# Optimization experiments

Measured on AMD Instinct MI355X. Metric: run time of the kernel, lower is better.

## Reference

```python
import jax, jax.numpy as jnp
import numpy as np

INF8 = 255
H, D = 8, 64  # num_heads, head dim (hidden=512)
G = 1         # num_global_node


def setup_inputs() -> dict:
    key = jax.random.key(0)
    ks = jax.random.split(key, 12)
    B, N, HID = 8, 1023, 512
    S = N + G
    inp = {
        'q': jax.random.normal(ks[0], (B, S, HID), jnp.float32),
        'k': jax.random.normal(ks[1], (B, S, HID), jnp.float32),
        'v': jax.random.normal(ks[2], (B, S, HID), jnp.float32),
        'attn_bias': jax.random.randint(ks[3], (B, N, N, 1), 0, 255).astype(jnp.int32),
        'Wq': 0.02 * jax.random.normal(ks[4], (HID, HID), jnp.float32),
        'bq': jnp.zeros((HID,), jnp.float32),
        'Wk': 0.02 * jax.random.normal(ks[5], (HID, HID), jnp.float32),
        'bk': jnp.zeros((HID,), jnp.float32),
        'Wv': 0.02 * jax.random.normal(ks[6], (HID, HID), jnp.float32),
        'bv': jnp.zeros((HID,), jnp.float32),
        'Wo': 0.02 * jax.random.normal(ks[7], (HID, HID), jnp.float32),
        'bo': jnp.zeros((HID,), jnp.float32),
        'bias_table': 0.02 * jax.random.normal(ks[8], (INF8 + 1, H), jnp.float32),
        'vbias': 0.02 * jax.random.normal(ks[9], (G, H), jnp.float32),
    }
    return inp


def _structural_bias(attn_bias, bias_table, vbias):
    # attn_bias: [B, N, N, 1] int -> [B, H, N+G, N+G] float
    ab = attn_bias[..., 0]                      # [B,N,N]
    B, N, _ = ab.shape
    bias = bias_table[ab]                       # [B,N,N,H]
    mask = ab == INF8
    bias = jnp.where(mask[..., None], -jnp.inf, bias)
    row = jnp.broadcast_to(vbias[None, :, None, :], (B, G, N, bias.shape[-1]))
    bias = jnp.concatenate([bias, row], axis=1)             # [B,N+G,N,H]
    col = jnp.broadcast_to(vbias[None, None, :, :], (B, N + G, G, bias.shape[-1]))
    bias = jnp.concatenate([bias, col], axis=2)             # [B,N+G,N+G,H]
    return bias.transpose(0, 3, 1, 2)                       # [B,H,S,S]


def reference(q, k, v, attn_bias, Wq, bq, Wk, bk, Wv, bv, Wo, bo, bias_table, vbias):
    B, S, HID = q.shape
    scale = D ** -0.5
    qh = (q @ Wq.T + bq).reshape(B, S, H, D)
    kh = (k @ Wk.T + bk).reshape(B, S, H, D)
    vh = (v @ Wv.T + bv).reshape(B, S, H, D)
    scores = jnp.einsum('bshd,bthd->bhst', qh * scale, kh)  # [B,H,S,S]
    scores = scores + _structural_bias(attn_bias, bias_table, vbias)
    p = jax.nn.softmax(scores, axis=-1)
    # dropout is identity in eval mode
    ctx = jnp.einsum('bhst,bthd->bshd', p, vh).reshape(B, S, HID)
    return ctx @ Wo.T + bo
```

## Files before the change

### kernel.cpp

```cpp
#include <hip/hip_runtime.h>
#include <hip/hip_bf16.h>


typedef __attribute__((ext_vector_type(8)))  __bf16 bf16x8;
typedef __attribute__((ext_vector_type(16))) float  f32x16;

__device__ inline f32x16 zero16(){
  f32x16 z;
  #pragma unroll
  for (int i=0;i<16;i++) z[i] = 0.0f;
  return z;
}

__device__ inline unsigned short f2bf(float x){
  unsigned u = __float_as_uint(x);
  u += 0x7fffu + ((u>>16)&1u);
  return (unsigned short)(u>>16);
}
__device__ inline unsigned f2bf_pair(float a, float b){
  unsigned ua = __float_as_uint(a); ua += 0x7fffu + ((ua>>16)&1u);
  unsigned ub = __float_as_uint(b); ub += 0x7fffu + ((ub>>16)&1u);
  return (ua>>16) | (ub & 0xffff0000u);
}
__device__ inline unsigned comb2(unsigned a, unsigned b, float rn){
  const float a0 = __uint_as_float(a<<16), a1 = __uint_as_float(a & 0xffff0000u);
  const float b0 = __uint_as_float(b<<16), b1 = __uint_as_float(b & 0xffff0000u);
  return f2bf_pair((a0+b0)*rn, (a1+b1)*rn);
}

__device__ inline void bar_lgkm(){
  asm volatile("s_waitcnt lgkmcnt(0)" ::: "memory");
  __builtin_amdgcn_s_barrier();
}

__global__ __launch_bounds__(256)
void ab_transpose(const int* ab, unsigned short* abT)
{
  __shared__ int tl[64*65];
  const int k  = blockIdx.x;
  const int b  = k >> 8;
  const int ti = k & 255;
  const int t0 = (ti & 15) << 6, q0 = (ti >> 4) << 6;
  const int c  = threadIdx.x & 63, r0 = threadIdx.x >> 6;
  #pragma unroll
  for (int rp = 0; rp < 16; ++rp){
    const int r = r0 + rp*4;
    const int q = q0 + r, t = t0 + c;
    int v = 256;
    if (q < 1023 && t < 1023) v = ab[((size_t)b*1023 + q)*1023 + t];
    tl[r*65 + c] = v;
  }
  __syncthreads();
  unsigned short* dst = abT + ((size_t)b << 20);
  #pragma unroll
  for (int rp = 0; rp < 16; ++rp){
    const int r = r0 + rp*4;
    dst[(size_t)(t0 + r)*1024 + q0 + c] = (unsigned short)tl[c*65 + r];
  }
}

__global__ __launch_bounds__(256)
void qkv_proj(const float* xq, const float* xk, const float* xv,
              const float* Wq, const float* Wk, const float* Wv,
              const float* bq, const float* bk, const float* bv,
              unsigned short* qh, unsigned short* kh, unsigned short* vht2,
              float scaleq)
{
  __shared__ unsigned short lda[128*40];
  __shared__ unsigned short ldb[128*40];
  const int bid = blockIdx.x;
  const int sel = bid >> 8;
  const int t   = bid & 255;
  const float *RA, *RB, *bias;
  int r0, c0;
  if (sel == 0){ RA = xq; RB = Wq; bias = bq; r0 = (t&63)*128; c0 = (t>>6)*128; }
  else if (sel == 1){ RA = xk; RB = Wk; bias = bk; r0 = (t&63)*128; c0 = (t>>6)*128; }
  else { RA = Wv; RB = xv; bias = bv; r0 = (t&3)*128; c0 = (t>>2)*128; }

  const int tid  = threadIdx.x;
  const int w    = tid>>6, lane = tid&63, lo = lane&31, hi = lane>>5;
  const int wr   = (w>>1)*64, wc = (w&1)*64;
  const int arow = tid>>1, kb = (tid&1)*16;

  f32x16 acc[2][2];
  #pragma unroll
  for (int i=0;i<2;i++)
    #pragma unroll
    for (int j=0;j<2;j++) acc[i][j] = zero16();

  float4 ra[4], rb4[4];
  {
    const float4* p = (const float4*)(RA + (r0+arow)*512 + kb);
    ra[0]=p[0]; ra[1]=p[1]; ra[2]=p[2]; ra[3]=p[3];
    const float4* pq = (const float4*)(RB + (c0+arow)*512 + kb);
    rb4[0]=pq[0]; rb4[1]=pq[1]; rb4[2]=pq[2]; rb4[3]=pq[3];
  }

  for (int ks=0; ks<16; ++ks){
    bar_lgkm();
    {
      uint4 w0, w1;
      w0.x = f2bf_pair(ra[0].x, ra[0].y); w0.y = f2bf_pair(ra[0].z, ra[0].w);
      w0.z = f2bf_pair(ra[1].x, ra[1].y); w0.w = f2bf_pair(ra[1].z, ra[1].w);
      w1.x = f2bf_pair(ra[2].x, ra[2].y); w1.y = f2bf_pair(ra[2].z, ra[2].w);
      w1.z = f2bf_pair(ra[3].x, ra[3].y); w1.w = f2bf_pair(ra[3].z, ra[3].w);
      uint4* pa = (uint4*)&lda[arow*40 + kb];
      pa[0] = w0; pa[1] = w1;
      uint4 v0, v1;
      v0.x = f2bf_pair(rb4[0].x, rb4[0].y); v0.y = f2bf_pair(rb4[0].z, rb4[0].w);
      v0.z = f2bf_pair(rb4[1].x, rb4[1].y); v0.w = f2bf_pair(rb4[1].z, rb4[1].w);
      v1.x = f2bf_pair(rb4[2].x, rb4[2].y); v1.y = f2bf_pair(rb4[2].z, rb4[2].w);
      v1.z = f2bf_pair(rb4[3].x, rb4[3].y); v1.w = f2bf_pair(rb4[3].z, rb4[3].w);
      uint4* pb = (uint4*)&ldb[arow*40 + kb];
      pb[0] = v0; pb[1] = v1;
    }
    if (ks < 15){
      const int k0 = (ks+1)*32;
      const float4* p = (const float4*)(RA + (r0+arow)*512 + k0 + kb);
      ra[0]=p[0]; ra[1]=p[1]; ra[2]=p[2]; ra[3]=p[3];
      const float4* pq = (const float4*)(RB + (c0+arow)*512 + k0 + kb);
      rb4[0]=pq[0]; rb4[1]=pq[1]; rb4[2]=pq[2]; rb4[3]=pq[3];
    }
    bar_lgkm();
    #pragma unroll
    for (int kf=0; kf<2; ++kf){
      bf16x8 af0 = *(const bf16x8*)&lda[(wr+lo)*40    + kf*16 + hi*8];
      bf16x8 af1 = *(const bf16x8*)&lda[(wr+32+lo)*40 + kf*16 + hi*8];
      bf16x8 bg0 = *(const bf16x8*)&ldb[(wc+lo)*40    + kf*16 + hi*8];
      bf16x8 bg1 = *(const bf16x8*)&ldb[(wc+32+lo)*40 + kf*16 + hi*8];
      acc[0][0] = __builtin_amdgcn_mfma_f32_32x32x16_bf16(af0, bg0, acc[0][0], 0,0,0);
      acc[0][1] = __builtin_amdgcn_mfma_f32_32x32x16_bf16(af0, bg1, acc[0][1], 0,0,0);
      acc[1][0] = __builtin_amdgcn_mfma_f32_32x32x16_bf16(af1, bg0, acc[1][0], 0,0,0);
      acc[1][1] = __builtin_amdgcn_mfma_f32_32x32x16_bf16(af1, bg1, acc[1][1], 0,0,0);
    }
  }

  #pragma unroll
  for (int mi=0;mi<2;mi++){
    #pragma unroll
    for (int ni=0;ni<2;ni++){
      #pragma unroll
      for (int r=0;r<16;r++){
        const int rl = wr + mi*32 + (r&3) + 8*(r>>2) + 4*hi;
        const int cl = wc + ni*32 + lo;
        const int rg = r0 + rl, cg = c0 + cl;
        float v = acc[mi][ni][r];
        if (sel == 0){
          v = (v + bias[cg]) * scaleq;
          const int bb = rg>>10, s = rg&1023, h = cg>>6, d = cg&63;
          qh[(((bb*8+h)*1024)+s)*64 + d] = f2bf(v);
        } else if (sel == 1){
          v = v + bias[cg];
          const int bb = rg>>10, s = rg&1023, h = cg>>6, d = cg&63;
          kh[(((bb*8+h)*1024)+s)*64 + d] = f2bf(v);
        } else {
          v = v + bias[rg];
          const int h = rg>>6, d = rg&63, bb = cg>>10, s = cg&1023;
          vht2[(((size_t)(bb*8+h)*32 + (s>>5))*64 + d)*32 + (s&31)] = f2bf(v);
        }
      }
    }
  }
}

__global__ __launch_bounds__(256)
void out_proj(const unsigned short* ctx0, const unsigned short* ctx1,
              const float* lsump, const float* Wo, const float* bo, float* OUT)
{
  __shared__ unsigned short lda[128*40];
  __shared__ unsigned short ldb[128*40];
  const int tid  = threadIdx.x;
  const int r0   = blockIdx.x*128, c0 = blockIdx.y*128;
  const int w    = tid>>6, lane = tid&63, lo = lane&31, hi = lane>>5;
  const int wr   = (w>>1)*64, wc = (w&1)*64;
  const int arow = tid>>1, kb = (tid&1)*16;
  const int rgs  = r0 + arow, bb = rgs>>10, ss = rgs&1023;
  const float* lb0 = lsump + (size_t)(bb*8)*1024 + ss;
  const float* lb1 = lsump + (size_t)((8+bb)*8)*1024 + ss;

  f32x16 acc[2][2];
  #pragma unroll
  for (int i=0;i<2;i++)
    #pragma unroll
    for (int j=0;j<2;j++) acc[i][j] = zero16();

  uint4 ra0[2], ra1[2];
  float4 rb4[4];
  float l0, l1;

  {
    const uint4* p0 = (const uint4*)(ctx0 + rgs*512 + kb);
    ra0[0]=p0[0]; ra0[1]=p0[1];
    const uint4* p1 = (const uint4*)(ctx1 + rgs*512 + kb);
    ra1[0]=p1[0]; ra1[1]=p1[1];
    const int h = kb>>6;
    l0 = lb0[h*1024]; l1 = lb1[h*1024];
    const float4* pq = (const float4*)(Wo + (c0+arow)*512 + kb);
    rb4[0]=pq[0]; rb4[1]=pq[1]; rb4[2]=pq[2]; rb4[3]=pq[3];
  }

  for (int ks=0; ks<16; ++ks){
    bar_lgkm();
    {
      const float rn = __builtin_amdgcn_rcpf(l0 + l1);
      uint4 w0, w1;
      w0.x = comb2(ra0[0].x, ra1[0].x, rn); w0.y = comb2(ra0[0].y, ra1[0].y, rn);
      w0.z = comb2(ra0[0].z, ra1[0].z, rn); w0.w = comb2(ra0[0].w, ra1[0].w, rn);
      w1.x = comb2(ra0[1].x, ra1[1].x, rn); w1.y = comb2(ra0[1].y, ra1[1].y, rn);
      w1.z = comb2(ra0[1].z, ra1[1].z, rn); w1.w = comb2(ra0[1].w, ra1[1].w, rn);
      uint4* pa = (uint4*)&lda[arow*40 + kb];
      pa[0] = w0; pa[1] = w1;
      uint4 v0, v1;
      v0.x = f2bf_pair(rb4[0].x, rb4[0].y); v0.y = f2bf_pair(rb4[0].z, rb4[0].w);
      v0.z = f2bf_pair(rb4[1].x, rb4[1].y); v0.w = f2bf_pair(rb4[1].z, rb4[1].w);
      v1.x = f2bf_pair(rb4[2].x, rb4[2].y); v1.y = f2bf_pair(rb4[2].z, rb4[2].w);
      v1.z = f2bf_pair(rb4[3].x, rb4[3].y); v1.w = f2bf_pair(rb4[3].z, rb4[3].w);
      uint4* pb = (uint4*)&ldb[arow*40 + kb];
      pb[0] = v0; pb[1] = v1;
    }
    if (ks < 15){
      const int k0 = (ks+1)*32;
      const uint4* p0 = (const uint4*)(ctx0 + rgs*512 + k0 + kb);
      ra0[0]=p0[0]; ra0[1]=p0[1];
      const uint4* p1 = (const uint4*)(ctx1 + rgs*512 + k0 + kb);
      ra1[0]=p1[0]; ra1[1]=p1[1];
      const int h = (k0+kb)>>6;
      l0 = lb0[h*1024]; l1 = lb1[h*1024];
      const float4* pq = (const float4*)(Wo + (c0+arow)*512 + k0 + kb);
      rb4[0]=pq[0]; rb4[1]=pq[1]; rb4[2]=pq[2]; rb4[3]=pq[3];
    }
    bar_lgkm();
    #pragma unroll
    for (int kf=0; kf<2; ++kf){
      bf16x8 af0 = *(const bf16x8*)&lda[(wr+lo)*40    + kf*16 + hi*8];
      bf16x8 af1 = *(const bf16x8*)&lda[(wr+32+lo)*40 + kf*16 + hi*8];
      bf16x8 bg0 = *(const bf16x8*)&ldb[(wc+lo)*40    + kf*16 + hi*8];
      bf16x8 bg1 = *(const bf16x8*)&ldb[(wc+32+lo)*40 + kf*16 + hi*8];
      acc[0][0] = __builtin_amdgcn_mfma_f32_32x32x16_bf16(af0, bg0, acc[0][0], 0,0,0);
      acc[0][1] = __builtin_amdgcn_mfma_f32_32x32x16_bf16(af0, bg1, acc[0][1], 0,0,0);
      acc[1][0] = __builtin_amdgcn_mfma_f32_32x32x16_bf16(af1, bg0, acc[1][0], 0,0,0);
      acc[1][1] = __builtin_amdgcn_mfma_f32_32x32x16_bf16(af1, bg1, acc[1][1], 0,0,0);
    }
  }

  #pragma unroll
  for (int mi=0;mi<2;mi++){
    #pragma unroll
    for (int ni=0;ni<2;ni++){
      #pragma unroll
      for (int r=0;r<16;r++){
        const int rl = wr + mi*32 + (r&3) + 8*(r>>2) + 4*hi;
        const int cl = wc + ni*32 + lo;
        const int rg = r0 + rl, cg = c0 + cl;
        OUT[rg*512 + cg] = acc[mi][ni][r] + bo[cg];
      }
    }
  }
}

__global__ __launch_bounds__(256)
void attn_fused(const unsigned short* qh, const unsigned short* kh,
                const unsigned short* vht2, const unsigned short* abT,
                const float* bias_table, const float* vbias,
                unsigned short* ctxp, float* lsump)
{
  __shared__ float tbl[260];
  __shared__ unsigned short kls[32*72];
  __shared__ unsigned short vls[64*40];
  __shared__ unsigned short abls[32*136];

  const int tid = threadIdx.x;
  const int m   = blockIdx.x;
  const int sg  = m >> 7;
  const int c   = m & 127;
  const int h   = c & 7;
  const int ts  = (c >> 3) & 1;
  const int b   = c >> 4;
  const int tb  = ts*512;
  const int q0  = sg*128;

  for (int i = tid; i < 257; i += 256){
    float v;
    if (i < 255)       v = bias_table[i*8 + h];
    else if (i == 255) v = -1.0e30f;
    else               v = vbias[h];
    tbl[i] = v * 1.4426950408889634f;
  }

  const int w = tid>>6, lane = tid&63, lo = lane&31, hi = lane>>5;
  const bool hib = (hi != 0);
  const int s0 = q0 + w*32;

  const unsigned short* qbase  = qh   + (size_t)(b*8+h)*65536;
  const unsigned short* kbase  = kh   + (size_t)(b*8+h)*65536 + (size_t)tb*64;
  const unsigned short* vbase  = vht2 + ((size_t)(b*8+h)*32 + (tb>>5))*2048;
  const unsigned short* abbase = abT  + ((size_t)b<<20) + q0;

  bf16x8 qf[4];
  #pragma unroll
  for (int kf=0; kf<4; ++kf)
    qf[kf] = *(const bf16x8*)&qbase[(s0+lo)*64 + kf*16 + hi*8];

  f32x16 accv[2]; accv[0] = zero16(); accv[1] = zero16();
  float lsum = 0.0f;

  const int kdst = (tid>>3)*72  + (tid&7)*8;
  const int vdst = (tid>>2)*40  + (tid&3)*8;
  const int adst = (tid>>3)*136 + (tid&7)*16;

  uint4 krg, vrg, ar0, ar1;
  krg = *(const uint4*)&kbase[tid*8];
  vrg = *(const uint4*)&vbase[tid*8];
  ar0 = *(const uint4*)&abbase[(size_t)(tb + (tid>>3))*1024 + (tid&7)*16];
  ar1 = *(const uint4*)&abbase[(size_t)(tb + (tid>>3))*1024 + (tid&7)*16 + 8];

  for (int tt=0; tt<512; tt+=32){
    bar_lgkm();
    *(uint4*)&kls[kdst]    = krg;
    *(uint4*)&vls[vdst]    = vrg;
    *(uint4*)&abls[adst]   = ar0;
    *(uint4*)&abls[adst+8] = ar1;
    {
      const int tn = (tt+32)&511;
      krg = *(const uint4*)&kbase[tn*64 + tid*8];
      vrg = *(const uint4*)&vbase[(tn>>5)*2048 + tid*8];
      ar0 = *(const uint4*)&abbase[(size_t)(tb + tn + (tid>>3))*1024 + (tid&7)*16];
      ar1 = *(const uint4*)&abbase[(size_t)(tb + tn + (tid>>3))*1024 + (tid&7)*16 + 8];
    }
    bar_lgkm();

    f32x16 sc = zero16();
    #pragma unroll
    for (int kf=0; kf<4; ++kf){
      bf16x8 kfr = *(const bf16x8*)&kls[lo*72 + kf*16 + hi*8];
      sc = __builtin_amdgcn_mfma_f32_32x32x16_bf16(kfr, qf[kf], sc, 0,0,0);
    }

    unsigned d[4][2];
    float ls = 0.0f;
    #pragma unroll
    for (int g=0; g<4; ++g){
      float p[4];
      #pragma unroll
      for (int u=0; u<4; ++u){
        const int crow = u + 8*g + 4*hi;
        const int idx  = abls[crow*136 + w*32 + lo];
        p[u] = __builtin_amdgcn_exp2f(sc[4*g+u] + tbl[idx]);
        ls  += p[u];
      }
      d[g][0] = f2bf_pair(p[0], p[1]);
      d[g][1] = f2bf_pair(p[2], p[3]);
    }
    lsum += ls;

    unsigned x[4][2];
    #pragma unroll
    for (int g=0; g<4; ++g){
      x[g][0] = __shfl_xor(d[g][0], 32, 64);
      x[g][1] = __shfl_xor(d[g][1], 32, 64);
    }

    #pragma unroll
    for (int c2=0; c2<2; ++c2){
      union { unsigned u[4]; bf16x8 v; } pc;
      pc.u[0] = hib ? x[2*c2+1][0] : d[2*c2][0];
      pc.u[1] = hib ? x[2*c2+1][1] : d[2*c2][1];
      pc.u[2] = hib ? d[2*c2+1][0] : x[2*c2][0];
      pc.u[3] = hib ? d[2*c2+1][1] : x[2*c2][1];
      bf16x8 vf0 = *(const bf16x8*)&vls[(     lo)*40 + c2*16 + hi*8];
      bf16x8 vf1 = *(const bf16x8*)&vls[(32 + lo)*40 + c2*16 + hi*8];
      accv[0] = __builtin_amdgcn_mfma_f32_32x32x16_bf16(pc.v, vf0, accv[0], 0,0,0);
      accv[1] = __builtin_amdgcn_mfma_f32_32x32x16_bf16(pc.v, vf1, accv[1], 0,0,0);
    }
  }

  lsum += __shfl_xor(lsum, 32, 64);

  unsigned short* cbase = ctxp + (size_t)ts*4194304;
  #pragma unroll
  for (int dc=0; dc<2; ++dc){
    #pragma unroll
    for (int r=0;r<16;r++){
      const int rq = (r&3) + 8*(r>>2) + 4*hi;
      cbase[((size_t)b*1024 + s0 + rq)*512 + h*64 + dc*32 + lo] = f2bf(accv[dc][r]);
    }
  }
  if (hi == 0){
    lsump[((size_t)(ts*8 + b)*8 + h)*1024 + s0 + lo] = lsum;
  }
}

extern "C" void kernel_launch(void* const* d_in, const int* in_sizes, int n_in,
                              void* d_out, int out_size, void* d_ws, size_t ws_size,
                              hipStream_t stream)
{
  const float* q    = (const float*)d_in[0];
  const float* k    = (const float*)d_in[1];
  const float* v    = (const float*)d_in[2];
  const int*   ab   = (const int*)  d_in[3];
  const float* Wq   = (const float*)d_in[4];
  const float* bq   = (const float*)d_in[5];
  const float* Wk   = (const float*)d_in[6];
  const float* bk   = (const float*)d_in[7];
  const float* Wv   = (const float*)d_in[8];
  const float* bv   = (const float*)d_in[9];
  const float* Wo   = (const float*)d_in[10];
  const float* bo   = (const float*)d_in[11];
  const float* btab = (const float*)d_in[12];
  const float* vbia = (const float*)d_in[13];

  char* ws = (char*)d_ws;
  unsigned short* qh   = (unsigned short*)(ws);
  unsigned short* kh   = (unsigned short*)(ws + ((size_t) 8<<20));
  unsigned short* vht2 = (unsigned short*)(ws + ((size_t)16<<20));
  unsigned short* ctxp = (unsigned short*)(ws + ((size_t)24<<20));
  float*          lsmp = (float*)         (ws + ((size_t)40<<20));
  unsigned short* abT  = (unsigned short*)(ws + ((size_t)41<<20));

  const float SCALE_Q = 0.125f * 1.4426950408889634f;

  qkv_proj<<<768, 256, 0, stream>>>(q, k, v, Wq, Wk, Wv, bq, bk, bv,
                                    qh, kh, vht2, SCALE_Q);
  ab_transpose<<<2048, 256, 0, stream>>>(ab, abT);
  attn_fused<<<1024, 256, 0, stream>>>(qh, kh, vht2, abT, btab, vbia,
                                       ctxp, lsmp);
  out_proj<<<dim3(64,4), 256, 0, stream>>>(ctxp, ctxp + (size_t)4194304,
                                           lsmp, Wo, bo, (float*)d_out);
}
```

Baseline: 128.4 us.

## Halve QKV projection tile width and double-buffer LDS staging

The QKV projection GEMM now uses 128x64 output tiles instead of 128x128, doubling the grid to 1536 blocks so the 256 CUs get better coverage. LDS is double-buffered with a two-deep register prefetch, so each k-step needs one barrier instead of two and the bf16 conversion and stores overlap the MFMA work. In exchange, each block reuses its A tile across fewer columns, so the activation rows are read from global memory twice as often.

```diff
diff --git a/kernel.cpp b/kernel.cpp
--- a/kernel.cpp
+++ b/kernel.cpp
@@ -66,98 +66,108 @@
               unsigned short* qh, unsigned short* kh, unsigned short* vht2,
               float scaleq)
 {
-  __shared__ unsigned short lda[128*40];
-  __shared__ unsigned short ldb[128*40];
+  __shared__ unsigned short lda[2][128*40];
+  __shared__ unsigned short ldb[2][64*40];
   const int bid = blockIdx.x;
-  const int sel = bid >> 8;
-  const int t   = bid & 255;
+  const int sel = bid >> 9;
+  const int t   = bid & 511;
   const float *RA, *RB, *bias;
   int r0, c0;
-  if (sel == 0){ RA = xq; RB = Wq; bias = bq; r0 = (t&63)*128; c0 = (t>>6)*128; }
-  else if (sel == 1){ RA = xk; RB = Wk; bias = bk; r0 = (t&63)*128; c0 = (t>>6)*128; }
-  else { RA = Wv; RB = xv; bias = bv; r0 = (t&3)*128; c0 = (t>>2)*128; }
+  if (sel == 0){ RA = xq; RB = Wq; bias = bq; r0 = (t&63)*128; c0 = (t>>6)*64; }
+  else if (sel == 1){ RA = xk; RB = Wk; bias = bk; r0 = (t&63)*128; c0 = (t>>6)*64; }
+  else { RA = Wv; RB = xv; bias = bv; r0 = (t&3)*128; c0 = (t>>2)*64; }
 
   const int tid  = threadIdx.x;
   const int w    = tid>>6, lane = tid&63, lo = lane&31, hi = lane>>5;
-  const int wr   = (w>>1)*64, wc = (w&1)*64;
-  const int arow = tid>>1, kb = (tid&1)*16;
-
-  f32x16 acc[2][2];
-  #pragma unroll
-  for (int i=0;i<2;i++)
-    #pragma unroll
-    for (int j=0;j<2;j++) acc[i][j] = zero16();
-
-  float4 ra[4], rb4[4];
+  const int wr   = (w>>1)*64, wc = (w&1)*32;
+  const int arow = tid>>1, kba = (tid&1)*16;
+  const int brow = tid>>2, kbb = (tid&3)*8;
+
+  f32x16 acc[2];
+  acc[0] = zero16(); acc[1] = zero16();
+
+  float4 ra[4], rb[2];
+
   {
-    const float4* p = (const float4*)(RA + (r0+arow)*512 + kb);
+    const float4* p = (const float4*)(RA + (r0+arow)*512 + kba);
     ra[0]=p[0]; ra[1]=p[1]; ra[2]=p[2]; ra[3]=p[3];
-    const float4* pq = (const float4*)(RB + (c0+arow)*512 + kb);
-    rb4[0]=pq[0]; rb4[1]=pq[1]; rb4[2]=pq[2]; rb4[3]=pq[3];
-  }
+    const float4* q4 = (const float4*)(RB + (c0+brow)*512 + kbb);
+    rb[0]=q4[0]; rb[1]=q4[1];
+  }
+  {
+    uint4 w0, w1;
+    w0.x = f2bf_pair(ra[0].x, ra[0].y); w0.y = f2bf_pair(ra[0].z, ra[0].w);
+    w0.z = f2bf_pair(ra[1].x, ra[1].y); w0.w = f2bf_pair(ra[1].z, ra[1].w);
+    w1.x = f2bf_pair(ra[2].x, ra[2].y); w1.y = f2bf_pair(ra[2].z, ra[2].w);
+    w1.z = f2bf_pair(ra[3].x, ra[3].y); w1.w = f2bf_pair(ra[3].z, ra[3].w);
+    uint4* pa = (uint4*)&lda[0][arow*40 + kba];
+    pa[0] = w0; pa[1] = w1;
+    uint4 v0;
+    v0.x = f2bf_pair(rb[0].x, rb[0].y); v0.y = f2bf_pair(rb[0].z, rb[0].w);
+    v0.z = f2bf_pair(rb[1].x, rb[1].y); v0.w = f2bf_pair(rb[1].z, rb[1].w);
+    *(uint4*)&ldb[0][brow*40 + kbb] = v0;
+  }
+  {
+    const float4* p = (const float4*)(RA + (r0+arow)*512 + 32 + kba);
+    ra[0]=p[0]; ra[1]=p[1]; ra[2]=p[2]; ra[3]=p[3];
+    const float4* q4 = (const float4*)(RB + (c0+brow)*512 + 32 + kbb);
+    rb[0]=q4[0]; rb[1]=q4[1];
+  }
+  bar_lgkm();
 
   for (int ks=0; ks<16; ++ks){
-    bar_lgkm();
-    {
+    const int cur = ks & 1;
+    if (ks < 15){
       uint4 w0, w1;
       w0.x = f2bf_pair(ra[0].x, ra[0].y); w0.y = f2bf_pair(ra[0].z, ra[0].w);
       w0.z = f2bf_pair(ra[1].x, ra[1].y); w0.w = f2bf_pair(ra[1].z, ra[1].w);
       w1.x = f2bf_pair(ra[2].x, ra[2].y); w1.y = f2bf_pair(ra[2].z, ra[2].w);
       w1.z = f2bf_pair(ra[3].x, ra[3].y); w1.w = f2bf_pair(ra[3].z, ra[3].w);
-      uint4* pa = (uint4*)&lda[arow*40 + kb];
+      uint4* pa = (uint4*)&lda[cur^1][arow*40 + kba];
       pa[0] = w0; pa[1] = w1;
-      uint4 v0, v1;
-      v0.x = f2bf_pair(rb4[0].x, rb4[0].y); v0.y = f2bf_pair(rb4[0].z, rb4[0].w);
-      v0.z = f2bf_pair(rb4[1].x, rb4[1].y); v0.w = f2bf_pair(rb4[1].z, rb4[1].w);
-      v1.x = f2bf_pair(rb4[2].x, rb4[2].y); v1.y = f2bf_pair(rb4[2].z, rb4[2].w);
-      v1.z = f2bf_pair(rb4[3].x, rb4[3].y); v1.w = f2bf_pair(rb4[3].z, rb4[3].w);
-      uint4* pb = (uint4*)&ldb[arow*40 + kb];
-      pb[0] = v0; pb[1] = v1;
-    }
-    if (ks < 15){
-      const int k0 = (ks+1)*32;
-      const float4* p = (const float4*)(RA + (r0+arow)*512 + k0 + kb);
+      uint4 v0;
+      v0.x = f2bf_pair(rb[0].x, rb[0].y); v0.y = f2bf_pair(rb[0].z, rb[0].w);
+      v0.z = f2bf_pair(rb[1].x, rb[1].y); v0.w = f2bf_pair(rb[1].z, rb[1].w);
+      *(uint4*)&ldb[cur^1][brow*40 + kbb] = v0;
+    }
+    if (ks < 14){
+      const int k0 = (ks+2)*32;
+      const float4* p = (const float4*)(RA + (r0+arow)*512 + k0 + kba);
       ra[0]=p[0]; ra[1]=p[1]; ra[2]=p[2]; ra[3]=p[3];
-      const float4* pq = (const float4*)(RB + (c0+arow)*512 + k0 + kb);
-      rb4[0]=pq[0]; rb4[1]=pq[1]; rb4[2]=pq[2]; rb4[3]=pq[3];
+      const float4* q4 = (const float4*)(RB + (c0+brow)*512 + k0 + kbb);
+      rb[0]=q4[0]; rb[1]=q4[1];
+    }
+    #pragma unroll
+    for (int kf=0; kf<2; ++kf){
+      bf16x8 af0 = *(const bf16x8*)&lda[cur][(wr+lo)*40    + kf*16 + hi*8];
+      bf16x8 af1 = *(const bf16x8*)&lda[cur][(wr+32+lo)*40 + kf*16 + hi*8];
+      bf16x8 bg0 = *(const bf16x8*)&ldb[cur][(wc+lo)*40    + kf*16 + hi*8];
+      acc[0] = __builtin_amdgcn_mfma_f32_32x32x16_bf16(af0, bg0, acc[0], 0,0,0);
+      acc[1] = __builtin_amdgcn_mfma_f32_32x32x16_bf16(af1, bg0, acc[1], 0,0,0);
     }
     bar_lgkm();
-    #pragma unroll
-    for (int kf=0; kf<2; ++kf){
-      bf16x8 af0 = *(const bf16x8*)&lda[(wr+lo)*40    + kf*16 + hi*8];
-      bf16x8 af1 = *(const bf16x8*)&lda[(wr+32+lo)*40 + kf*16 + hi*8];
-      bf16x8 bg0 = *(const bf16x8*)&ldb[(wc+lo)*40    + kf*16 + hi*8];
-      bf16x8 bg1 = *(const bf16x8*)&ldb[(wc+32+lo)*40 + kf*16 + hi*8];
-      acc[0][0] = __builtin_amdgcn_mfma_f32_32x32x16_bf16(af0, bg0, acc[0][0], 0,0,0);
-      acc[0][1] = __builtin_amdgcn_mfma_f32_32x32x16_bf16(af0, bg1, acc[0][1], 0,0,0);
-      acc[1][0] = __builtin_amdgcn_mfma_f32_32x32x16_bf16(af1, bg0, acc[1][0], 0,0,0);
-      acc[1][1] = __builtin_amdgcn_mfma_f32_32x32x16_bf16(af1, bg1, acc[1][1], 0,0,0);
-    }
   }
 
   #pragma unroll
   for (int mi=0;mi<2;mi++){
     #pragma unroll
-    for (int ni=0;ni<2;ni++){
-      #pragma unroll
-      for (int r=0;r<16;r++){
-        const int rl = wr + mi*32 + (r&3) + 8*(r>>2) + 4*hi;
-        const int cl = wc + ni*32 + lo;
-        const int rg = r0 + rl, cg = c0 + cl;
-        float v = acc[mi][ni][r];
-        if (sel == 0){
-          v = (v + bias[cg]) * scaleq;
-          const int bb = rg>>10, s = rg&1023, h = cg>>6, d = cg&63;
-          qh[(((bb*8+h)*1024)+s)*64 + d] = f2bf(v);
-        } else if (sel == 1){
-          v = v + bias[cg];
-          const int bb = rg>>10, s = rg&1023, h = cg>>6, d = cg&63;
-          kh[(((bb*8+h)*1024)+s)*64 + d] = f2bf(v);
-        } else {
-          v = v + bias[rg];
-          const int h = rg>>6, d = rg&63, bb = cg>>10, s = cg&1023;
-          vht2[(((size_t)(bb*8+h)*32 + (s>>5))*64 + d)*32 + (s&31)] = f2bf(v);
-        }
+    for (int r=0;r<16;r++){
+      const int rl = wr + mi*32 + (r&3) + 8*(r>>2) + 4*hi;
+      const int cl = wc + lo;
+      const int rg = r0 + rl, cg = c0 + cl;
+      float v = acc[mi][r];
+      if (sel == 0){
+        v = (v + bias[cg]) * scaleq;
+        const int bb = rg>>10, s = rg&1023, h = cg>>6, d = cg&63;
+        qh[(((bb*8+h)*1024)+s)*64 + d] = f2bf(v);
+      } else if (sel == 1){
+        v = v + bias[cg];
+        const int bb = rg>>10, s = rg&1023, h = cg>>6, d = cg&63;
+        kh[(((bb*8+h)*1024)+s)*64 + d] = f2bf(v);
+      } else {
+        v = v + bias[rg];
+        const int h = rg>>6, d = rg&63, bb = cg>>10, s = cg&1023;
+        vht2[(((size_t)(bb*8+h)*32 + (s>>5))*64 + d)*32 + (s&31)] = f2bf(v);
       }
     }
   }
@@ -419,8 +429,8 @@
 
   const float SCALE_Q = 0.125f * 1.4426950408889634f;
 
-  qkv_proj<<<768, 256, 0, stream>>>(q, k, v, Wq, Wk, Wv, bq, bk, bv,
-                                    qh, kh, vht2, SCALE_Q);
+  qkv_proj<<<1536, 256, 0, stream>>>(q, k, v, Wq, Wk, Wv, bq, bk, bv,
+                                     qh, kh, vht2, SCALE_Q);
   ab_transpose<<<2048, 256, 0, stream>>>(ab, abT);
   attn_fused<<<1024, 256, 0, stream>>>(qh, kh, vht2, abT, btab, vbia,
                                        ctxp, lsmp);
```

After: 132.5 us. +3.2%, slower.
